# Kernel tuning notes

Measured on AMD Instinct MI355X. Metric: run time of the kernel, lower is better.

Reference implementation:

```python
import jax, jax.numpy as jnp
from jax import lax
from jax.scipy.special import logsumexp
import numpy as np

B, T, V, K = 64, 512, 40, 15
CE, CH, WH, WE = 128, 256, 256, 768  # char emb, char hidden, word hidden, word emb dims


def setup_inputs() -> dict:
    key = jax.random.key(0)
    ks = iter(jax.random.split(key, 40))
    def nrm(shape, s=0.05):
        return jax.random.normal(next(ks), shape, jnp.float32) * s
    char_ids = jax.random.randint(next(ks), (B, T), 0, V)
    word_embeddings = jax.random.normal(next(ks), (B, T, WE), jnp.float32)
    tags = jax.random.randint(next(ks), (B, T), 0, K)
    emb = nrm((V, CE), 1.0).at[0].set(0.0)  # padding_idx=0
    inp = dict(char_ids=char_ids, word_embeddings=word_embeddings, tags=tags, char_emb_table=emb)
    # LSTM weights stacked over directions: Wih (2,4H,in), Whh (2,4H,H), b (2,4H)
    inp.update(
        c0_Wih=nrm((2, 4 * CH, CE)), c0_Whh=nrm((2, 4 * CH, CH)), c0_bih=nrm((2, 4 * CH)), c0_bhh=nrm((2, 4 * CH)),
        c1_Wih=nrm((2, 4 * CH, 2 * CH)), c1_Whh=nrm((2, 4 * CH, CH)), c1_bih=nrm((2, 4 * CH)), c1_bhh=nrm((2, 4 * CH)),
        w0_Wih=nrm((2, 4 * WH, WE)), w0_Whh=nrm((2, 4 * WH, WH)), w0_bih=nrm((2, 4 * WH)), w0_bhh=nrm((2, 4 * WH)),
        w1_Wih=nrm((2, 4 * WH, 2 * WH)), w1_Whh=nrm((2, 4 * WH, WH)), w1_bih=nrm((2, 4 * WH)), w1_bhh=nrm((2, 4 * WH)),
        cls_w1=nrm((512, 1024)), cls_b1=nrm((512,)), cls_w2=nrm((K, 512)), cls_b2=nrm((K,)),
        crf_start=nrm((K,), 0.1), crf_end=nrm((K,), 0.1), crf_trans=nrm((K, K), 0.1))
    return inp


def _lstm_dir(x, Wih, Whh, bih, bhh, reverse):
    # x: (B,T,D) -> (B,T,H). PyTorch gate order: i,f,g,o.
    xT = jnp.swapaxes(x, 0, 1)  # (T,B,D)
    if reverse:
        xT = jnp.flip(xT, 0)
    xg = jnp.einsum('tbd,gd->tbg', xT, Wih) + bih + bhh  # (T,B,4H)
    H = Whh.shape[1]
    Bn = x.shape[0]
    def step(carry, g_in):
        h, c = carry
        g = g_in + h @ Whh.T
        i, f, gc, o = jnp.split(g, 4, -1)
        c = jax.nn.sigmoid(f) * c + jax.nn.sigmoid(i) * jnp.tanh(gc)
        h = jax.nn.sigmoid(o) * jnp.tanh(c)
        return (h, c), h
    z = jnp.zeros((Bn, H), x.dtype)
    _, hs = lax.scan(step, (z, z), xg)
    if reverse:
        hs = jnp.flip(hs, 0)
    return jnp.swapaxes(hs, 0, 1)


def _bilayer(x, Wih, Whh, bih, bhh):
    f = _lstm_dir(x, Wih[0], Whh[0], bih[0], bhh[0], False)
    b = _lstm_dir(x, Wih[1], Whh[1], bih[1], bhh[1], True)
    return jnp.concatenate([f, b], -1)


def _crf_nll(emissions, tags, start, end, trans):
    # torchcrf forward with reduction='mean', full mask; loss = -llh.mean()
    em = jnp.swapaxes(emissions, 0, 1)  # (T,B,K)
    tg = jnp.swapaxes(tags, 0, 1)       # (T,B)
    num = start[tg[0]] + jnp.take_along_axis(em[0], tg[0][:, None], 1)[:, 0]
    num = num + trans[tg[:-1], tg[1:]].sum(0)
    num = num + jnp.take_along_axis(em[1:], tg[1:][..., None], -1)[..., 0].sum(0)
    num = num + end[tg[-1]]
    def step(score, e):
        s = logsumexp(score[:, :, None] + trans[None] + e[:, None, :], axis=1)
        return s, None
    score, _ = lax.scan(step, start[None] + em[0], em[1:])
    denom = logsumexp(score + end[None], axis=-1)
    return -(num - denom).mean()


def reference(char_ids, word_embeddings, tags, char_emb_table,
              c0_Wih, c0_Whh, c0_bih, c0_bhh, c1_Wih, c1_Whh, c1_bih, c1_bhh,
              w0_Wih, w0_Whh, w0_bih, w0_bhh, w1_Wih, w1_Whh, w1_bih, w1_bhh,
              cls_w1, cls_b1, cls_w2, cls_b2, crf_start, crf_end, crf_trans):
    ce = char_emb_table[char_ids]  # (B,T,128)
    ch = _bilayer(ce, c0_Wih, c0_Whh, c0_bih, c0_bhh)
    ch = _bilayer(ch, c1_Wih, c1_Whh, c1_bih, c1_bhh)  # (B,T,512), dropout is eval-mode identity
    wh = _bilayer(word_embeddings, w0_Wih, w0_Whh, w0_bih, w0_bhh)
    wh = _bilayer(wh, w1_Wih, w1_Whh, w1_bih, w1_bhh)  # (B,T,512)
    comb = jnp.concatenate([ch, wh], -1)  # (B,T,1024)
    h = jax.nn.relu(comb @ cls_w1.T + cls_b1)
    logits = h @ cls_w2.T + cls_b2  # (B,T,15)
    return _crf_nll(logits, tags, crf_start, crf_end, crf_trans)
```

## Files before the change

kernel.cpp:

```cpp
#include <hip/hip_runtime.h>

#define DEVI __device__ __forceinline__

typedef __attribute__((ext_vector_type(8))) __bf16 bf16x8;
typedef __attribute__((ext_vector_type(4))) float f32x4;

DEVI unsigned short f2b(float f) {
  unsigned u = __float_as_uint(f);
  u = u + 0x7fffu + ((u >> 16) & 1u);
  return (unsigned short)(u >> 16);
}
DEVI float lo16(unsigned u) { return __uint_as_float(u << 16); }
DEVI float hi16(unsigned u) { return __uint_as_float(u & 0xffff0000u); }
#if __has_builtin(__builtin_amdgcn_rcpf)
DEVI float rcpf(float x) { return __builtin_amdgcn_rcpf(x); }
#else
DEVI float rcpf(float x) { return 1.f / x; }
#endif
DEVI float sigm(float x) { return rcpf(1.f + __expf(-x)); }

#if __has_builtin(__builtin_amdgcn_cvt_pk_fp8_f32)
DEVI unsigned char f2e4m3(float f) {
  return (unsigned char)(__builtin_amdgcn_cvt_pk_fp8_f32(f, f, 0, false) & 0xff);
}
#else
DEVI unsigned char f2e4m3(float f) {
  unsigned u = __float_as_uint(f);
  unsigned s = (u >> 31) << 7;
  float a = fabsf(f);
  if (a >= 448.f) return (unsigned char)(s | 0x7e);
  if (a < 0.015625f) {
    int m = (int)rintf(a * 512.f);
    if (m >= 8) return (unsigned char)(s | 0x08);
    return (unsigned char)(s | m);
  }
  unsigned ur = u + 0x7FFFF + ((u >> 20) & 1);
  int e8 = (int)((ur >> 23) & 255) - 127 + 7;
  unsigned m3 = (ur >> 20) & 7;
  if (e8 > 15 || (e8 == 15 && m3 > 6)) return (unsigned char)(s | 0x7e);
  if (e8 <= 0) return (unsigned char)s;
  return (unsigned char)(s | (e8 << 3) | m3);
}
#endif

__global__ void cvt_bf16(const float* __restrict__ in, unsigned short* __restrict__ out, int n) {
  for (int i = blockIdx.x * blockDim.x + threadIdx.x; i < n; i += gridDim.x * blockDim.x)
    out[i] = f2b(in[i]);
}

__global__ void whh_pack(const float* __restrict__ W, uint2* __restrict__ out) {
  int idx = blockIdx.x * blockDim.x + threadIdx.x;
  if (idx >= 65536) return;
  int d = idx >> 15, rem = idx & 32767;
  int mt = rem >> 9, kf = (rem >> 6) & 7, lane = rem & 63;
  int row = mt * 16 + (lane & 15);
  int unit = row >> 2, gate = row & 3;
  int kb = kf * 32 + (lane >> 4) * 8;
  const float* w = W + (((size_t)d * 1024 + gate * 256 + unit) * 256 + kb);
  unsigned lo = 0, hi = 0;
  #pragma unroll
  for (int j = 0; j < 4; ++j) lo |= (unsigned)f2e4m3(w[j]) << (8 * j);
  #pragma unroll
  for (int j = 0; j < 4; ++j) hi |= (unsigned)f2e4m3(w[4 + j]) << (8 * j);
  out[idx] = make_uint2(lo, hi);
}

__global__ void bias_sum(const float* __restrict__ a, const float* __restrict__ b,
                         float* __restrict__ o, int n) {
  int i = blockIdx.x * blockDim.x + threadIdx.x;
  if (i < n) o[i] = a[i] + b[i];
}

__global__ void embed_gather(const int* __restrict__ ids, const float* __restrict__ tab,
                             unsigned short* __restrict__ out, int total) {
  for (int i = blockIdx.x * blockDim.x + threadIdx.x; i < total; i += gridDim.x * blockDim.x) {
    int bt = i >> 7, c = i & 127;
    out[i] = f2b(tab[(size_t)ids[bt] * 128 + c]);
  }
}

template <int ACT, int PERM>
__global__ __launch_bounds__(256) void gemm_lds(const unsigned short* __restrict__ A, int lda,
                                                const unsigned short* __restrict__ W,
                                                const float* __restrict__ bias,
                                                unsigned short* __restrict__ C,
                                                int M, int N, int K) {
  const int ntiles = N >> 7;
  const int mt = blockIdx.x / ntiles;
  const int nt = blockIdx.x - mt * ntiles;
  const int m0 = mt << 7, n0 = nt << 7;
  const int tid = threadIdx.x;
  const int w = tid >> 6, lane = tid & 63, r = lane & 15, q = lane >> 4;
  __shared__ unsigned short lsA[4096], lsB[4096];
  f32x4 acc[16];
  #pragma unroll
  for (int i = 0; i < 16; ++i) acc[i] = f32x4{0.f, 0.f, 0.f, 0.f};

  const int srow = tid >> 2, sq = tid & 3;
  const int s0 = (srow << 2) | (sq ^ (srow & 3) ^ ((srow >> 2) & 3));
  const unsigned short* gA = A + (size_t)(m0 + srow) * lda + sq * 8;
  const unsigned short* gB = W + (size_t)(n0 + srow) * K + sq * 8;
  const size_t gAs = (size_t)64 * lda, gBs = (size_t)64 * K;
  const int sw = q ^ (r & 3) ^ ((r >> 2) & 3);

  for (int k0 = 0; k0 < K; k0 += 32) {
    uint4 va0 = *(const uint4*)(gA + k0);
    uint4 va1 = *(const uint4*)(gA + gAs + k0);
    uint4 vb0 = *(const uint4*)(gB + k0);
    uint4 vb1 = *(const uint4*)(gB + gBs + k0);
    *(uint4*)(lsA + s0 * 8) = va0;
    *(uint4*)(lsA + s0 * 8 + 2048) = va1;
    *(uint4*)(lsB + s0 * 8) = vb0;
    *(uint4*)(lsB + s0 * 8 + 2048) = vb1;
    __syncthreads();
    const bf16x8 a0 = *(const bf16x8*)(const void*)(lsA + ((w * 32 + r) * 4 + sw) * 8);
    const bf16x8 a1 = *(const bf16x8*)(const void*)(lsA + ((w * 32 + 16 + r) * 4 + sw) * 8);
    #pragma unroll
    for (int nf = 0; nf < 8; ++nf) {
      const bf16x8 b = *(const bf16x8*)(const void*)(lsB + ((nf * 16 + r) * 4 + sw) * 8);
      acc[nf]     = __builtin_amdgcn_mfma_f32_16x16x32_bf16(a0, b, acc[nf], 0, 0, 0);
      acc[8 + nf] = __builtin_amdgcn_mfma_f32_16x16x32_bf16(a1, b, acc[8 + nf], 0, 0, 0);
    }
    __syncthreads();
  }
  #pragma unroll
  for (int mf = 0; mf < 2; ++mf) {
    const int rbase = m0 + w * 32 + mf * 16 + q * 4;
    #pragma unroll
    for (int nf = 0; nf < 8; ++nf) {
      const f32x4 a = acc[mf * 8 + nf];
      const int col = n0 + nf * 16 + r;
      const float bv = bias[col];
      int oc = col;
      if constexpr (PERM) oc = (col & 1024) | ((col & 255) << 2) | ((col >> 8) & 3);
      #pragma unroll
      for (int i = 0; i < 4; ++i) {
        float v = a[i] + bv;
        if constexpr (ACT) v = fmaxf(v, 0.f);
        C[(size_t)(rbase + i) * N + oc] = f2b(v);
      }
    }
  }
}

__global__ __launch_bounds__(1024, 4) void lstm_mfma(
    const uint2* __restrict__ W0, const unsigned short* __restrict__ x0,
    unsigned short* __restrict__ o0, int oo0,
    const uint2* __restrict__ W1, const unsigned short* __restrict__ x1,
    unsigned short* __restrict__ o1, int oo1, int T) {
  const int bid = blockIdx.x;
  const int sg = bid & 3, dir = (bid >> 2) & 1, grp = bid >> 3;
  const uint2* __restrict__ Wp = (grp ? W1 : W0) + (size_t)dir * 32768;
  const unsigned short* __restrict__ xg = grp ? x1 : x0;
  unsigned short* __restrict__ out = grp ? o1 : o0;
  const int outOff = grp ? oo1 : oo0;

  const int tid = threadIdx.x;
  const int w = tid >> 6, lane = tid & 63, q = lane >> 4, n = lane & 15;
  const int b = sg * 16 + n;

  __shared__ long hb[2][512];
  __shared__ unsigned short hout[2][16][264];
  hb[0][tid & 511] = 0;
  hb[1][tid & 511] = 0;

  float c[4] = {0.f, 0.f, 0.f, 0.f};
  const unsigned short* xb = xg + ((size_t)b * T) * 2048 + dir * 1024 + (w * 16 + q) * 4;
  const uint2* wbase = Wp + (size_t)(w * 32) * 64 + lane;
  unsigned short* orow = out + ((size_t)(sg * 16 + w) * T) * 1024 + outOff + dir * 256 + lane * 4;

  const int tstep = dir ? -1 : 1;
  int t = dir ? T - 1 : 0;
  uint2 xv[4];
  #pragma unroll
  for (int j = 0; j < 4; ++j)
    xv[j] = *(const uint2*)(xb + (size_t)t * 2048 + j * 16);
  __syncthreads();

  int cur = 0;
  for (int ti = 0; ti < T; ++ti) {
    if (ti) {
      const uint2 hv = *(const uint2*)&hout[cur][w][lane * 4];
      *(uint2*)(orow + (size_t)(t - tstep) * 1024) = hv;
    }
    uint2 xn[4];
    if (ti + 1 < T) {
      #pragma unroll
      for (int j = 0; j < 4; ++j)
        xn[j] = *(const uint2*)(xb + (size_t)(t + tstep) * 2048 + j * 16);
    }
    f32x4 acc[4];
    #pragma unroll
    for (int j = 0; j < 4; ++j) acc[j] = f32x4{0.f, 0.f, 0.f, 0.f};
    #pragma unroll
    for (int kf = 0; kf < 8; ++kf) {
      const long bf = hb[cur][kf * 64 + q * 16 + n];
      #pragma unroll
      for (int j = 0; j < 4; ++j) {
        const long a = __builtin_bit_cast(long, wbase[(size_t)(j * 8 + kf) * 64]);
        acc[j] = __builtin_amdgcn_mfma_f32_16x16x32_fp8_fp8(a, bf, acc[j], 0, 0, 0);
      }
    }
    unsigned char* hw = (unsigned char*)&hb[cur ^ 1][0];
    #pragma unroll
    for (int j = 0; j < 4; ++j) {
      const int u = w * 16 + j * 4 + q;
      float gi = acc[j][0] + lo16(xv[j].x);
      float gf = acc[j][1] + hi16(xv[j].x);
      float gg = acc[j][2] + lo16(xv[j].y);
      float go = acc[j][3] + hi16(xv[j].y);
      gi = fminf(fmaxf(gi, -20.f), 20.f);
      gf = fminf(fmaxf(gf, -20.f), 20.f);
      gg = fminf(fmaxf(gg, -10.f), 10.f);
      go = fminf(fmaxf(go, -20.f), 20.f);
      const float Ei = __expf(-gi), Ef = __expf(-gf), G = __expf(2.f * gg);
      const float P = (1.f + Ei) * (G + 1.f);
      const float num = fmaf(c[j], P, (G - 1.f) * (1.f + Ef));
      c[j] = num * rcpf((1.f + Ef) * P);
      const float cc = fminf(fmaxf(c[j], -15.f), 15.f);
      const float x2 = __expf(-2.f * cc), Eo = __expf(-go);
      const float h = (1.f - x2) * rcpf((1.f + x2) * (1.f + Eo));
      hw[(u >> 3) * 128 + n * 8 + (u & 7)] = f2e4m3(h);
      hout[cur ^ 1][n][u] = f2b(h);
    }
    __syncthreads();
    #pragma unroll
    for (int j = 0; j < 4; ++j) xv[j] = xn[j];
    t += tstep;
    cur ^= 1;
  }
  const uint2 hv = *(const uint2*)&hout[cur][w][lane * 4];
  *(uint2*)(orow + (size_t)(t - tstep) * 1024) = hv;
}

__global__ __launch_bounds__(256) void cls2_kernel(const unsigned short* __restrict__ h1,
                                                   const unsigned short* __restrict__ w2,
                                                   const float* __restrict__ b2,
                                                   float* __restrict__ logits, int M) {
  int idx = blockIdx.x * 256 + threadIdx.x;
  int row = idx >> 4, n = idx & 15;
  if (row >= M || n >= 15) return;
  const unsigned* hp = (const unsigned*)(h1 + (size_t)row * 512);
  const unsigned* wp = (const unsigned*)(w2 + (size_t)n * 512);
  float acc = 0.f;
  #pragma unroll 8
  for (int k = 0; k < 256; ++k) {
    unsigned uh = hp[k], uw = wp[k];
    acc = fmaf(lo16(uh), lo16(uw), acc);
    acc = fmaf(hi16(uh), hi16(uw), acc);
  }
  logits[(size_t)row * 16 + n] = acc + b2[n];
}

__global__ __launch_bounds__(256) void crf_num(const float* __restrict__ logits,
                                               const int* __restrict__ tags,
                                               const float* __restrict__ start,
                                               const float* __restrict__ end,
                                               const float* __restrict__ trans,
                                               float* __restrict__ numout, int T) {
  int b = blockIdx.x, tid = threadIdx.x;
  const int* tg = tags + (size_t)b * T;
  float s = 0.f;
  for (int t = tid; t < T; t += 256) {
    int cur = tg[t];
    s += logits[((size_t)b * T + t) * 16 + cur];
    if (t > 0) s += trans[tg[t - 1] * 15 + cur];
  }
  #pragma unroll
  for (int off = 32; off > 0; off >>= 1) s += __shfl_down(s, off, 64);
  __shared__ float red[4];
  if ((tid & 63) == 0) red[tid >> 6] = s;
  __syncthreads();
  if (tid == 0)
    numout[b] = red[0] + red[1] + red[2] + red[3] + start[tg[0]] + end[tg[T - 1]];
}

__global__ void crf_denom(const float* __restrict__ logits, const float* __restrict__ start,
                          const float* __restrict__ end, const float* __restrict__ trans,
                          float* __restrict__ denout, int T) {
  int b = blockIdx.x;
  int lane = threadIdx.x;
  int kp = lane < 15 ? lane : 0;
  float tcol[15];
  #pragma unroll
  for (int k = 0; k < 15; ++k) tcol[k] = trans[k * 15 + kp];
  float score = start[kp] + logits[((size_t)b * T) * 16 + kp];
  for (int t = 1; t < T; ++t) {
    float e = logits[((size_t)b * T + t) * 16 + kp];
    float s[15], m = -3.4e38f;
    #pragma unroll
    for (int k = 0; k < 15; ++k) {
      s[k] = __shfl(score, k, 64) + tcol[k];
      m = fmaxf(m, s[k]);
    }
    float sum = 0.f;
    #pragma unroll
    for (int k = 0; k < 15; ++k) sum += __expf(s[k] - m);
    score = e + m + __logf(sum);
  }
  float x = score + end[kp];
  float m = -3.4e38f;
  #pragma unroll
  for (int k = 0; k < 15; ++k) m = fmaxf(m, __shfl(x, k, 64));
  float sum = 0.f;
  #pragma unroll
  for (int k = 0; k < 15; ++k) sum += __expf(__shfl(x, k, 64) - m);
  if (lane == 0) denout[b] = m + __logf(sum);
}

__global__ void crf_final(const float* __restrict__ num, const float* __restrict__ den,
                          float* __restrict__ out) {
  int l = threadIdx.x;
  float v = den[l] - num[l];
  #pragma unroll
  for (int off = 32; off > 0; off >>= 1) v += __shfl_xor(v, off, 64);
  if (l == 0) out[0] = v * (1.f / 64.f);
}

extern "C" void kernel_launch(void* const* d_in, const int* in_sizes, int n_in,
                              void* d_out, int out_size, void* d_ws, size_t ws_size,
                              hipStream_t stream) {
  const int B = 64, T = 512, M = B * T;
  const float* we   = (const float*)d_in[1];
  const int*   cid  = (const int*)d_in[0];
  const int*   tags = (const int*)d_in[2];
  const float* etab = (const float*)d_in[3];

  char* ws = (char*)d_ws;
  size_t off = 0;
  auto alloc = [&](size_t bytes) -> char* {
    char* p = ws + off;
    off += (bytes + 255) & ~(size_t)255;
    return p;
  };
  unsigned short* wih_c0 = (unsigned short*)alloc((size_t)2048 * 128 * 2);
  unsigned short* wih_c1 = (unsigned short*)alloc((size_t)2048 * 512 * 2);
  unsigned short* wih_w0 = (unsigned short*)alloc((size_t)2048 * 768 * 2);
  unsigned short* wih_w1 = (unsigned short*)alloc((size_t)2048 * 512 * 2);
  unsigned short* cls1b  = (unsigned short*)alloc((size_t)512 * 1024 * 2);
  unsigned short* cls2b  = (unsigned short*)alloc((size_t)15 * 512 * 2);
  uint2* whh_c0 = (uint2*)alloc((size_t)65536 * 8);
  uint2* whh_c1 = (uint2*)alloc((size_t)65536 * 8);
  uint2* whh_w0 = (uint2*)alloc((size_t)65536 * 8);
  uint2* whh_w1 = (uint2*)alloc((size_t)65536 * 8);
  float* bs_c0 = (float*)alloc(2048 * 4);
  float* bs_c1 = (float*)alloc(2048 * 4);
  float* bs_w0 = (float*)alloc(2048 * 4);
  float* bs_w1 = (float*)alloc(2048 * 4);
  float* numb = (float*)alloc(64 * 4);
  float* denb = (float*)alloc(64 * 4);
  unsigned short* comb = (unsigned short*)alloc((size_t)M * 1024 * 2);
  unsigned short* xg_c = (unsigned short*)alloc((size_t)M * 2048 * 2);
  const size_t xgw_bytes = (size_t)M * 2048 * 2;
  const bool fused = (off + xgw_bytes) <= ws_size;
  unsigned short* xg_w;
  unsigned short* ce_b;
  unsigned short* we_b;
  if (fused) {
    xg_w = (unsigned short*)alloc(xgw_bytes);
    ce_b = xg_w;
    we_b = comb;
  } else {
    xg_w = xg_c;
    ce_b = (unsigned short*)alloc((size_t)M * 128 * 2);
    we_b = (unsigned short*)alloc((size_t)M * 768 * 2);
  }
  unsigned short* h1 = xg_c;
  float* logits = (float*)(xg_c + (size_t)24 * 1024 * 1024);

  cvt_bf16<<<1024, 256, 0, stream>>>((const float*)d_in[4],  wih_c0, 2048 * 128);
  cvt_bf16<<<1024, 256, 0, stream>>>((const float*)d_in[8],  wih_c1, 2048 * 512);
  cvt_bf16<<<1024, 256, 0, stream>>>((const float*)d_in[12], wih_w0, 2048 * 768);
  cvt_bf16<<<1024, 256, 0, stream>>>((const float*)d_in[16], wih_w1, 2048 * 512);
  cvt_bf16<<<1024, 256, 0, stream>>>((const float*)d_in[20], cls1b, 512 * 1024);
  cvt_bf16<<<64, 256, 0, stream>>>((const float*)d_in[22], cls2b, 15 * 512);
  cvt_bf16<<<4096, 256, 0, stream>>>(we, we_b, M * 768);
  whh_pack<<<256, 256, 0, stream>>>((const float*)d_in[5],  whh_c0);
  whh_pack<<<256, 256, 0, stream>>>((const float*)d_in[9],  whh_c1);
  whh_pack<<<256, 256, 0, stream>>>((const float*)d_in[13], whh_w0);
  whh_pack<<<256, 256, 0, stream>>>((const float*)d_in[17], whh_w1);
  bias_sum<<<8, 256, 0, stream>>>((const float*)d_in[6],  (const float*)d_in[7],  bs_c0, 2048);
  bias_sum<<<8, 256, 0, stream>>>((const float*)d_in[10], (const float*)d_in[11], bs_c1, 2048);
  bias_sum<<<8, 256, 0, stream>>>((const float*)d_in[14], (const float*)d_in[15], bs_w0, 2048);
  bias_sum<<<8, 256, 0, stream>>>((const float*)d_in[18], (const float*)d_in[19], bs_w1, 2048);
  embed_gather<<<8192, 256, 0, stream>>>(cid, etab, ce_b, M * 128);

  const int G2048 = (M >> 7) * (2048 >> 7);
  const int G512  = (M >> 7) * (512 >> 7);
  if (fused) {
    gemm_lds<0, 1><<<G2048, 256, 0, stream>>>(ce_b, 128, wih_c0, bs_c0, xg_c, M, 2048, 128);
    gemm_lds<0, 1><<<G2048, 256, 0, stream>>>(we_b, 768, wih_w0, bs_w0, xg_w, M, 2048, 768);
    lstm_mfma<<<16, 1024, 0, stream>>>(whh_c0, xg_c, comb, 0,
                                       whh_w0, xg_w, comb, 512, T);
    gemm_lds<0, 1><<<G2048, 256, 0, stream>>>(comb, 1024, wih_c1, bs_c1, xg_c, M, 2048, 512);
    gemm_lds<0, 1><<<G2048, 256, 0, stream>>>(comb + 512, 1024, wih_w1, bs_w1, xg_w, M, 2048, 512);
    lstm_mfma<<<16, 1024, 0, stream>>>(whh_c1, xg_c, comb, 0,
                                       whh_w1, xg_w, comb, 512, T);
  } else {
    gemm_lds<0, 1><<<G2048, 256, 0, stream>>>(ce_b, 128, wih_c0, bs_c0, xg_c, M, 2048, 128);
    lstm_mfma<<<8, 1024, 0, stream>>>(whh_c0, xg_c, comb, 0, whh_c0, xg_c, comb, 0, T);
    gemm_lds<0, 1><<<G2048, 256, 0, stream>>>(comb, 1024, wih_c1, bs_c1, xg_c, M, 2048, 512);
    lstm_mfma<<<8, 1024, 0, stream>>>(whh_c1, xg_c, comb, 0, whh_c1, xg_c, comb, 0, T);
    gemm_lds<0, 1><<<G2048, 256, 0, stream>>>(we_b, 768, wih_w0, bs_w0, xg_c, M, 2048, 768);
    lstm_mfma<<<8, 1024, 0, stream>>>(whh_w0, xg_c, comb, 512, whh_w0, xg_c, comb, 512, T);
    gemm_lds<0, 1><<<G2048, 256, 0, stream>>>(comb + 512, 1024, wih_w1, bs_w1, xg_c, M, 2048, 512);
    lstm_mfma<<<8, 1024, 0, stream>>>(whh_w1, xg_c, comb, 512, whh_w1, xg_c, comb, 512, T);
  }
  gemm_lds<1, 0><<<G512, 256, 0, stream>>>(comb, 1024, cls1b, (const float*)d_in[21], h1, M, 512, 1024);
  cls2_kernel<<<2048, 256, 0, stream>>>(h1, cls2b, (const float*)d_in[23], logits, M);
  crf_num<<<64, 256, 0, stream>>>(logits, tags, (const float*)d_in[24], (const float*)d_in[25],
                                  (const float*)d_in[26], numb, T);
  crf_denom<<<64, 64, 0, stream>>>(logits, (const float*)d_in[24], (const float*)d_in[25],
                                   (const float*)d_in[26], denb, T);
  crf_final<<<1, 64, 0, stream>>>(numb, denb, (float*)d_out);
}
```

Measured before the change: 4.164 ms.

## Cache half of recurrent FP8 weights in LDS and simplify gate math

Result: slower. 7.346 ms (+76.4%).

```diff
diff --git a/kernel.cpp b/kernel.cpp
--- a/kernel.cpp
+++ b/kernel.cpp
@@ -18,6 +18,7 @@
 DEVI float rcpf(float x) { return 1.f / x; }
 #endif
 DEVI float sigm(float x) { return rcpf(1.f + __expf(-x)); }
+DEVI float tanh_f(float x) { return fmaf(2.f, rcpf(1.f + __expf(-2.f * x)), -1.f); }
 
 #if __has_builtin(__builtin_amdgcn_cvt_pk_fp8_f32)
 DEVI unsigned char f2e4m3(float f) {
@@ -161,12 +162,18 @@
 
   __shared__ long hb[2][512];
   __shared__ unsigned short hout[2][16][264];
+  __shared__ long wlds[16384];
   hb[0][tid & 511] = 0;
   hb[1][tid & 511] = 0;
+  if (w < 8) {
+    const uint2* ap = Wp + (size_t)(w * 32) * 64 + lane;
+    #pragma unroll
+    for (int i = 0; i < 32; ++i)
+      wlds[w * 2048 + i * 64 + lane] = __builtin_bit_cast(long, ap[(size_t)i * 64]);
+  }
 
   float c[4] = {0.f, 0.f, 0.f, 0.f};
   const unsigned short* xb = xg + ((size_t)b * T) * 2048 + dir * 1024 + (w * 16 + q) * 4;
-  const uint2* wbase = Wp + (size_t)(w * 32) * 64 + lane;
   unsigned short* orow = out + ((size_t)(sg * 16 + w) * T) * 1024 + outOff + dir * 256 + lane * 4;
 
   const int tstep = dir ? -1 : 1;
@@ -192,34 +199,37 @@
     f32x4 acc[4];
     #pragma unroll
     for (int j = 0; j < 4; ++j) acc[j] = f32x4{0.f, 0.f, 0.f, 0.f};
-    #pragma unroll
-    for (int kf = 0; kf < 8; ++kf) {
-      const long bf = hb[cur][kf * 64 + q * 16 + n];
+    if (w < 8) {
+      const long* wl = wlds + w * 2048 + lane;
       #pragma unroll
-      for (int j = 0; j < 4; ++j) {
-        const long a = __builtin_bit_cast(long, wbase[(size_t)(j * 8 + kf) * 64]);
-        acc[j] = __builtin_amdgcn_mfma_f32_16x16x32_fp8_fp8(a, bf, acc[j], 0, 0, 0);
+      for (int kf = 0; kf < 8; ++kf) {
+        const long bf = hb[cur][kf * 64 + q * 16 + n];
+        #pragma unroll
+        for (int j = 0; j < 4; ++j)
+          acc[j] = __builtin_amdgcn_mfma_f32_16x16x32_fp8_fp8(wl[(j * 8 + kf) * 64], bf, acc[j], 0, 0, 0);
+      }
+    } else {
+      const uint2* wg = Wp + (size_t)(w * 32) * 64 + lane;
+      #pragma unroll
+      for (int kf = 0; kf < 8; ++kf) {
+        const long bf = hb[cur][kf * 64 + q * 16 + n];
+        #pragma unroll
+        for (int j = 0; j < 4; ++j) {
+          const long a = __builtin_bit_cast(long, wg[(size_t)(j * 8 + kf) * 64]);
+          acc[j] = __builtin_amdgcn_mfma_f32_16x16x32_fp8_fp8(a, bf, acc[j], 0, 0, 0);
+        }
       }
     }
     unsigned char* hw = (unsigned char*)&hb[cur ^ 1][0];
     #pragma unroll
     for (int j = 0; j < 4; ++j) {
       const int u = w * 16 + j * 4 + q;
-      float gi = acc[j][0] + lo16(xv[j].x);
-      float gf = acc[j][1] + hi16(xv[j].x);
-      float gg = acc[j][2] + lo16(xv[j].y);
-      float go = acc[j][3] + hi16(xv[j].y);
-      gi = fminf(fmaxf(gi, -20.f), 20.f);
-      gf = fminf(fmaxf(gf, -20.f), 20.f);
-      gg = fminf(fmaxf(gg, -10.f), 10.f);
-      go = fminf(fmaxf(go, -20.f), 20.f);
-      const float Ei = __expf(-gi), Ef = __expf(-gf), G = __expf(2.f * gg);
-      const float P = (1.f + Ei) * (G + 1.f);
-      const float num = fmaf(c[j], P, (G - 1.f) * (1.f + Ef));
-      c[j] = num * rcpf((1.f + Ef) * P);
-      const float cc = fminf(fmaxf(c[j], -15.f), 15.f);
-      const float x2 = __expf(-2.f * cc), Eo = __expf(-go);
-      const float h = (1.f - x2) * rcpf((1.f + x2) * (1.f + Eo));
+      const float gi = acc[j][0] + lo16(xv[j].x);
+      const float gf = acc[j][1] + hi16(xv[j].x);
+      const float gg = acc[j][2] + lo16(xv[j].y);
+      const float go = acc[j][3] + hi16(xv[j].y);
+      c[j] = sigm(gf) * c[j] + sigm(gi) * tanh_f(gg);
+      const float h = sigm(go) * tanh_f(c[j]);
       hw[(u >> 3) * 128 + n * 8 + (u & 7)] = f2e4m3(h);
       hout[cur ^ 1][n][u] = f2b(h);
     }
```
